# Performance work log

Measured on AMD Instinct MI355X. Metric: run time of the kernel, lower is better.

## Reference

```python
import jax, jax.numpy as jnp
import numpy as np
import math

HIDDEN = 1024
N_HEADS = 16
HEAD_DIM = HIDDEN // N_HEADS

def _safe(x, clamp_val):
    x = jnp.nan_to_num(x, nan=0.0, posinf=0.0, neginf=0.0)
    return jnp.clip(x, -clamp_val, clamp_val)

def _stable_linear(x, W, b):
    # StableLinear: clamp(50) -> linear -> clamp(50)
    x = _safe(x, 50.0)
    out = x @ W.T + b
    return _safe(out, 50.0)

def setup_inputs() -> dict:
    key = jax.random.key(0)
    ks = jax.random.split(key, 12)
    bsz, q_len, kv_len = 4, 1024, 2048
    q = jax.random.normal(ks[0], (bsz, q_len, HIDDEN), dtype=jnp.float32)
    kv = jax.random.normal(ks[1], (bsz, kv_len, HIDDEN), dtype=jnp.float32)
    key_padding_mask = jax.random.bernoulli(ks[2], 0.1, (bsz, kv_len))
    bound = 1.0 / math.sqrt(HIDDEN)
    def mk_w(k):
        return jax.random.uniform(k, (HIDDEN, HIDDEN), jnp.float32, -bound, bound)
    def mk_b(k):
        return jax.random.uniform(k, (HIDDEN,), jnp.float32, -bound, bound)
    return {
        'q': q, 'kv': kv, 'key_padding_mask': key_padding_mask,
        'Wq': mk_w(ks[3]), 'bq': mk_b(ks[4]),
        'Wk': mk_w(ks[5]), 'bk': mk_b(ks[6]),
        'Wv': mk_w(ks[7]), 'bv': mk_b(ks[8]),
        'Wo': mk_w(ks[9]), 'bo': mk_b(ks[10]),
    }

def reference(q, kv, key_padding_mask, Wq, bq, Wk, bk, Wv, bv, Wo, bo):
    bsz, q_len, _ = q.shape
    kv_len = kv.shape[1]
    # outer _safe(50) then StableLinear's own _safe(50) (idempotent)
    qh = _stable_linear(_safe(q, 50.0), Wq, bq)
    kh = _stable_linear(_safe(kv, 50.0), Wk, bk)
    vh = _stable_linear(_safe(kv, 50.0), Wv, bv)
    # [b, h, s, d]
    qh = qh.reshape(bsz, q_len, N_HEADS, HEAD_DIM).transpose(0, 2, 1, 3)
    kh = kh.reshape(bsz, kv_len, N_HEADS, HEAD_DIM).transpose(0, 2, 1, 3)
    vh = vh.reshape(bsz, kv_len, N_HEADS, HEAD_DIM).transpose(0, 2, 1, 3)
    scores = jnp.einsum('bhqd,bhkd->bhqk', qh.astype(jnp.float32), kh.astype(jnp.float32))
    scores = scores / math.sqrt(HEAD_DIM)
    scores = jnp.clip(scores, -80.0, 80.0)
    scores = jnp.where(key_padding_mask[:, None, None, :], -10000.0, scores)
    attn = jax.nn.softmax(scores, axis=-1)  # dropout is identity in eval mode
    out = jnp.einsum('bhqk,bhkd->bhqd', attn, vh.astype(jnp.float32))
    out = out.transpose(0, 2, 1, 3).reshape(bsz, q_len, HIDDEN)
    out = _stable_linear(_safe(out, 50.0), Wo, bo)
    return _safe(out, 50.0)
```

## Files before the change

kernel.cpp:

```cpp
#include <hip/hip_runtime.h>
#include <hip/hip_bf16.h>
#include <stdint.h>
#include <math.h>

#define HIDDEN 1024
#define NHEADS 16
#define HDIM   64
#define BSZ    4
#define QLEN   1024
#define KVLEN  2048

typedef __bf16 bf16_t;
typedef __bf16 bf16x8 __attribute__((ext_vector_type(8)));
typedef __bf16 bf16x4 __attribute__((ext_vector_type(4)));
typedef float  f32x4  __attribute__((ext_vector_type(4)));

#define C_SCALE 0.18033688f
#define C_FMADD (-43.2808512f)

#define GLOAD16(g, l) \
    __builtin_amdgcn_global_load_lds((const __attribute__((address_space(1))) void*)(g), \
                                     (__attribute__((address_space(3))) void*)(l), 16, 0, 0)

__device__ __forceinline__ float clamp50(float v) {
    return fminf(fmaxf(v, -50.f), 50.f);
}

#define NQ4  ((BSZ * QLEN  * HIDDEN) / 4)
#define NKV4 ((BSZ * KVLEN * HIDDEN) / 4)
#define NW4  ((HIDDEN * HIDDEN) / 4)
#define NCVT ((NQ4 + NKV4 + 4 * NW4) / 256)

__global__ void cvt_all_kernel(const float* __restrict__ q, const float* __restrict__ kv,
                               const float* __restrict__ W0, const float* __restrict__ W1,
                               const float* __restrict__ W2, const float* __restrict__ W3,
                               bf16_t* __restrict__ q_bf, bf16_t* __restrict__ kv_bf,
                               bf16_t* __restrict__ w_bf,
                               const void* __restrict__ msk, float* __restrict__ maskadd) {
    if (blockIdx.x >= NCVT) {
        __shared__ int s_float, s_multi;
        const int t = threadIdx.x;
        if (t == 0) { s_float = 0; s_multi = 0; }
        __syncthreads();
        const uint32_t* w = (const uint32_t*)msk;
        int cf = 0, cm = 0;
        for (int i = t; i < 2048; i += 256) {
            uint32_t v = w[i];
            if (v == 0x3F800000u) cf++;
            else if (v & 0xFFFFFF00u) cm++;
        }
        if (cf) atomicAdd(&s_float, cf);
        if (cm) atomicAdd(&s_multi, cm);
        __syncthreads();
        const int mode = (s_float > 0) ? 2 : ((s_multi > 0) ? 0 : 1);
        const int base = (blockIdx.x - NCVT) * 2048;
        for (int i = base + t; i < base + 2048; i += 256) {
            bool m;
            if (mode == 2)      m = ((const float*)msk)[i] != 0.0f;
            else if (mode == 1) m = ((const int*)msk)[i] != 0;
            else                m = ((const unsigned char*)msk)[i] != 0;
            maskadd[i] = m ? (-100000.0f + C_FMADD) : C_FMADD;
        }
        return;
    }
    const int i = blockIdx.x * blockDim.x + threadIdx.x;
    const float4* src;
    bf16x4* dst;
    if (i < NQ4) {
        src = (const float4*)q + i;            dst = (bf16x4*)q_bf + i;
    } else if (i < NQ4 + NKV4) {
        const int j = i - NQ4;
        src = (const float4*)kv + j;           dst = (bf16x4*)kv_bf + j;
    } else {
        const int j = i - (NQ4 + NKV4);
        const int ws = j >> 18, off = j & (NW4 - 1);
        const float* W = (ws == 0) ? W0 : (ws == 1) ? W1 : (ws == 2) ? W2 : W3;
        src = (const float4*)W + off;          dst = (bf16x4*)w_bf + (size_t)ws * NW4 + off;
    }
    const float4 v = *src;
    bf16x4 o;
    o[0] = (bf16_t)clamp50(v.x); o[1] = (bf16_t)clamp50(v.y);
    o[2] = (bf16_t)clamp50(v.z); o[3] = (bf16_t)clamp50(v.w);
    *dst = o;
}

template <int NT>
__device__ __forceinline__ void stage_tile8(const char* __restrict__ Ab,
                                            const char* __restrict__ Bb,
                                            char* base, int kt, int wave, int rowl, int srcsw)
{
#pragma unroll
    for (int i = 0; i < 2; ++i) {
        const int row = i * 64 + wave * 8 + rowl;
        GLOAD16(Ab + (size_t)row * (HIDDEN * 2) + kt * 128 + srcsw,
                base + i * 8192 + wave * 1024);
    }
#pragma unroll
    for (int i = 0; i < NT / 64; ++i) {
        const int row = i * 64 + wave * 8 + rowl;
        GLOAD16(Bb + (size_t)row * (HIDDEN * 2) + kt * 128 + srcsw,
                base + 16384 + i * 8192 + wave * 1024);
    }
}

template <int NT>
__device__ __forceinline__ void gemm_core_db8(const char* __restrict__ Ab,
                                              const char* __restrict__ Bb,
                                              char* Ls,
                                              f32x4 (&acc)[4][NT / 64],
                                              int wave, int lane, int wm, int wn)
{
    constexpr int NFB = NT / 64;
    constexpr int BUF = (128 + NT) * 128;
    const int srcsw = ((lane & 7) ^ (lane >> 3)) << 4;
    const int rowl = lane >> 3;
    const int ql = lane & 15;

    stage_tile8<NT>(Ab, Bb, Ls, 0, wave, rowl, srcsw);
    __syncthreads();

    for (int kt = 0; kt < HIDDEN / 64; ++kt) {
        const int cur = kt & 1;
        if (kt < HIDDEN / 64 - 1)
            stage_tile8<NT>(Ab, Bb, Ls + (cur ^ 1) * BUF, kt + 1, wave, rowl, srcsw);
        const char* Abase = Ls + cur * BUF;
        const char* Bbase = Abase + 16384;
#pragma unroll
        for (int kc = 0; kc < 2; ++kc) {
            const int kbyte = kc * 64 + ((lane >> 4) << 4);
            bf16x8 af[4], bfr[NFB];
#pragma unroll
            for (int f2 = 0; f2 < 4; ++f2) {
                const int arow = wm * 64 + f2 * 16 + ql;
                af[f2] = *(const bf16x8*)(Abase + arow * 128 + (kbyte ^ ((arow & 7) << 4)));
            }
#pragma unroll
            for (int f2 = 0; f2 < NFB; ++f2) {
                const int brow = wn * (NT / 4) + f2 * 16 + ql;
                bfr[f2] = *(const bf16x8*)(Bbase + brow * 128 + (kbyte ^ ((brow & 7) << 4)));
            }
#pragma unroll
            for (int mf = 0; mf < 4; ++mf)
#pragma unroll
                for (int nf = 0; nf < NFB; ++nf)
                    acc[mf][nf] = __builtin_amdgcn_mfma_f32_16x16x32_bf16(af[mf], bfr[nf], acc[mf][nf], 0, 0, 0);
        }
        __syncthreads();
    }
}

template <int NF>
__device__ __forceinline__ void epi_head(f32x4 (&acc)[4][NF], const float* bias,
                                         bf16_t* out, int m0, int n0, int slog,
                                         int wm, int wn, int lane)
{
#pragma unroll
    for (int mf = 0; mf < 4; ++mf) {
#pragma unroll
        for (int nf = 0; nf < NF; ++nf) {
            const int gn = n0 + wn * (NF * 16) + nf * 16 + (lane & 15);
            const float bv = bias[gn];
#pragma unroll
            for (int r = 0; r < 4; ++r) {
                const int gm = m0 + wm * 64 + mf * 16 + ((lane >> 4) << 2) + r;
                const float v = clamp50(acc[mf][nf][r] + bv);
                const int b = gm >> slog;
                const int s = gm & ((1 << slog) - 1);
                const int h = gn >> 6, d = gn & 63;
                out[((((size_t)(b * NHEADS + h)) << slog) + s) * HDIM + d] = (bf16_t)v;
            }
        }
    }
}

__global__ __launch_bounds__(512)
void gemm_proj_all(const bf16_t* __restrict__ q_bf, const bf16_t* __restrict__ kv_bf,
                   const bf16_t* __restrict__ w_bf,
                   const float* __restrict__ bq, const float* __restrict__ bk,
                   const float* __restrict__ bv,
                   bf16_t* __restrict__ qh, bf16_t* __restrict__ kh,
                   bf16_t* __restrict__ vt)
{
    __shared__ __align__(16) bf16_t Smem[2 * 256 * 64];

    const int bid = blockIdx.x;
    const int lid = (bid & 7) * 160 + (bid >> 3);

    int seg, j;
    if (lid < 256)      { seg = 0; j = lid; }
    else if (lid < 768) { seg = 1; j = lid - 256; }
    else                { seg = 2; j = lid - 768; }
    const int m0 = (j >> 3) * 128;
    const int n0 = (j & 7) * 128;
    const bf16_t* A    = (seg == 0) ? q_bf : kv_bf;
    const bf16_t* B    = w_bf + (size_t)seg * (HIDDEN * HIDDEN);
    const float*  bias = (seg == 0) ? bq : (seg == 1) ? bk : bv;

    const int t = threadIdx.x;
    const int wave = t >> 6, lane = t & 63;
    const int wm = wave >> 2, wn = wave & 3;

    f32x4 acc[4][2] = {};
    gemm_core_db8<128>((const char*)A + (size_t)m0 * (HIDDEN * 2),
                       (const char*)B + (size_t)n0 * (HIDDEN * 2),
                       (char*)Smem, acc, wave, lane, wm, wn);

    if (seg == 0) {
        epi_head<2>(acc, bias, qh, m0, n0, 10, wm, wn, lane);
        return;
    }
    if (seg == 1) {
        epi_head<2>(acc, bias, kh, m0, n0, 11, wm, wn, lane);
        return;
    }

    bf16_t* Cls = Smem;
    const int dl = t >> 2;
    const int sh = (t & 3) << 4;
    const int gn = n0 + dl;
    const int h = gn >> 6, d = gn & 63;
    const int bb = m0 >> 11;
    bf16_t* dst = vt + ((size_t)((bb * NHEADS + h) * HDIM + d)) * KVLEN
                + (m0 & (KVLEN - 1)) + sh;
    __syncthreads();
#pragma unroll
    for (int ph = 0; ph < 2; ++ph) {
        if (wm == ph) {
#pragma unroll
            for (int mf = 0; mf < 4; ++mf) {
#pragma unroll
                for (int nf = 0; nf < 2; ++nf) {
                    const int dcol = wn * 32 + nf * 16 + (lane & 15);
                    const float bv2 = bias[n0 + dcol];
#pragma unroll
                    for (int r = 0; r < 4; ++r) {
                        const int srow = mf * 16 + ((lane >> 4) << 2) + r;
                        Cls[srow * 130 + dcol] = (bf16_t)clamp50(acc[mf][nf][r] + bv2);
                    }
                }
            }
        }
        __syncthreads();
#pragma unroll
        for (int j0 = 0; j0 < 16; j0 += 8) {
            bf16x8 v;
#pragma unroll
            for (int jj = 0; jj < 8; ++jj) v[jj] = Cls[(sh + j0 + jj) * 130 + dl];
            *(bf16x8*)(dst + ph * 64 + j0) = v;
        }
        __syncthreads();
    }
}

__global__ __launch_bounds__(512)
void gemm_out_kernel(const bf16_t* __restrict__ A, const bf16_t* __restrict__ B,
                     const float* __restrict__ bias, float* __restrict__ out)
{
    constexpr int NT = 64;
    __shared__ __align__(16) bf16_t Smem[2 * (128 + NT) * 64];

    const int bid = blockIdx.x;
    const int lid = (bid & 7) * 64 + (bid >> 3);
    const int m0 = (lid >> 4) * 128;
    const int n0 = (lid & 15) * NT;
    const int t = threadIdx.x;
    const int wave = t >> 6, lane = t & 63;
    const int wm = wave >> 2, wn = wave & 3;

    f32x4 acc[4][1] = {};
    gemm_core_db8<NT>((const char*)A + (size_t)m0 * (HIDDEN * 2),
                      (const char*)B + (size_t)n0 * (HIDDEN * 2),
                      (char*)Smem, acc, wave, lane, wm, wn);

#pragma unroll
    for (int mf = 0; mf < 4; ++mf) {
        const int gn = n0 + wn * 16 + (lane & 15);
        const float bv = bias[gn];
#pragma unroll
        for (int r = 0; r < 4; ++r) {
            const int gm = m0 + wm * 64 + mf * 16 + ((lane >> 4) << 2) + r;
            out[(size_t)gm * HIDDEN + gn] = clamp50(acc[mf][0][r] + bv);
        }
    }
}

__global__ __launch_bounds__(512)
void attn_fwd_kernel(const bf16_t* __restrict__ Qh, const bf16_t* __restrict__ Kh,
                     const bf16_t* __restrict__ Vt, const float* __restrict__ maskadd,
                     bf16_t* __restrict__ aout)
{
    __shared__ __align__(16) bf16_t Kls[2][64 * 64];
    __shared__ __align__(16) bf16_t Vls[2][64 * 64];
    __shared__ __align__(16) float Cbuf[4][32 * 64];
    __shared__ float Lbuf[4][2][16];

    const int f = blockIdx.x;
    const int o = (f & 7) * 64 + (f >> 3);
    const int qt = o & 7;
    const int bh = o >> 3;
    const int b = bh >> 4, h = bh & 15;
    const int t = threadIdx.x, wave = t >> 6, lane = t & 63;
    const int wq = wave & 3;
    const int wg = wave >> 2;
    const int g = lane >> 4, ql = lane & 15;

    const int qbase = qt * 128 + wq * 32;
    bf16x8 qf[2][2];
#pragma unroll
    for (int qq = 0; qq < 2; ++qq) {
        const bf16_t* qp = Qh + ((size_t)bh * QLEN + qbase + qq * 16 + ql) * HDIM + (g << 3);
        qf[qq][0] = *(const bf16x8*)qp;
        qf[qq][1] = *(const bf16x8*)(qp + 32);
    }

    f32x4 oacc[2][4] = {};
    float lsum[2] = {0.f, 0.f};

    const int srcsw = ((lane & 7) ^ (lane >> 3)) << 4;
    const int R = wave * 8 + (lane >> 3);
    const int kap = 32 * (R >> 5) + 8 * ((R >> 2) & 3) + 4 * ((R >> 4) & 1) + (R & 3);

    const char* Kb = (const char*)(Kh + (size_t)bh * KVLEN * HDIM);
    const char* Vb = (const char*)(Vt + (size_t)bh * HDIM * KVLEN);
    const float* mrow = maskadd + b * KVLEN + wg * 32 + g * 8;
    const int kb0 = g << 4;
    const int vcol = wg * 64 + kb0;

    GLOAD16(Kb + (size_t)kap * 128 + srcsw, (char*)&Kls[0][0] + wave * 1024);
    GLOAD16(Vb + (size_t)R * (KVLEN * 2) + srcsw, (char*)&Vls[0][0] + wave * 1024);
    f32x4 madd_c[2], madd_n[2];
    madd_c[0] = *(const f32x4*)(mrow);
    madd_c[1] = *(const f32x4*)(mrow + 4);
    __syncthreads();

    for (int kt = 0; kt < KVLEN / 64; ++kt) {
        const int cur = kt & 1;
        if (kt < KVLEN / 64 - 1) {
            const size_t ko = (size_t)(kt + 1) * 8192;
            GLOAD16(Kb + ko + (size_t)kap * 128 + srcsw,
                    (char*)&Kls[cur ^ 1][0] + wave * 1024);
            GLOAD16(Vb + (size_t)R * (KVLEN * 2) + (size_t)(kt + 1) * 128 + srcsw,
                    (char*)&Vls[cur ^ 1][0] + wave * 1024);
            madd_n[0] = *(const f32x4*)(mrow + (kt + 1) * 64);
            madd_n[1] = *(const f32x4*)(mrow + (kt + 1) * 64 + 4);
        }
        const char* Kc = (const char*)&Kls[cur][0];
        const char* Vc = (const char*)&Vls[cur][0];

        f32x4 sacc[2][2] = {};
        __builtin_amdgcn_s_setprio(1);
#pragma unroll
        for (int kb = 0; kb < 2; ++kb) {
            const int key = wg * 32 + kb * 16 + ql;
            const int rowoff = key * 128;
            const int sw = (key & 7) << 4;
            const bf16x8 kf0 = *(const bf16x8*)(Kc + rowoff + ((kb0)      ^ sw));
            const bf16x8 kf1 = *(const bf16x8*)(Kc + rowoff + ((kb0 + 64) ^ sw));
#pragma unroll
            for (int qq = 0; qq < 2; ++qq) {
                sacc[qq][kb] = __builtin_amdgcn_mfma_f32_16x16x32_bf16(kf0, qf[qq][0], sacc[qq][kb], 0, 0, 0);
                sacc[qq][kb] = __builtin_amdgcn_mfma_f32_16x16x32_bf16(kf1, qf[qq][1], sacc[qq][kb], 0, 0, 0);
            }
        }
        __builtin_amdgcn_s_setprio(0);

        bf16x8 pa[2];
#pragma unroll
        for (int qq = 0; qq < 2; ++qq) {
            float pv[2][4];
            float ls = 0.f;
#pragma unroll
            for (int kb = 0; kb < 2; ++kb) {
#pragma unroll
                for (int r = 0; r < 4; ++r) {
                    pv[kb][r] = __builtin_amdgcn_exp2f(
                        __builtin_fmaf(sacc[qq][kb][r], C_SCALE, madd_c[kb][r]));
                    ls += pv[kb][r];
                }
            }
            lsum[qq] += ls;
#pragma unroll
            for (int r = 0; r < 4; ++r) {
                pa[qq][r]     = (bf16_t)pv[0][r];
                pa[qq][4 + r] = (bf16_t)pv[1][r];
            }
        }

        __builtin_amdgcn_s_setprio(1);
#pragma unroll
        for (int db = 0; db < 4; ++db) {
            const int vrow = db * 16 + ql;
            const int vsw = (vrow & 7) << 4;
            const bf16x8 vf = *(const bf16x8*)(Vc + vrow * 128 + (vcol ^ vsw));
#pragma unroll
            for (int qq = 0; qq < 2; ++qq)
                oacc[qq][db] = __builtin_amdgcn_mfma_f32_16x16x32_bf16(pa[qq], vf, oacc[qq][db], 0, 0, 0);
        }
        __builtin_amdgcn_s_setprio(0);

        __syncthreads();
#pragma unroll
        for (int kb = 0; kb < 2; ++kb) madd_c[kb] = madd_n[kb];
    }

#pragma unroll
    for (int qq = 0; qq < 2; ++qq) {
        float l = lsum[qq];
        l += __shfl_xor(l, 16);
        l += __shfl_xor(l, 32);
        lsum[qq] = l;
    }
    const int rbase = g << 2;
    if (wg == 1) {
#pragma unroll
        for (int qq = 0; qq < 2; ++qq) {
#pragma unroll
            for (int db = 0; db < 4; ++db)
#pragma unroll
                for (int r = 0; r < 4; ++r)
                    Cbuf[wq][(qq * 16 + rbase + r) * 64 + db * 16 + ql] = oacc[qq][db][r];
            if (lane < 16) Lbuf[wq][qq][lane] = lsum[qq];
        }
    }
    __syncthreads();
    if (wg == 0) {
#pragma unroll
        for (int qq = 0; qq < 2; ++qq) {
            const float Lq = lsum[qq] + Lbuf[wq][qq][ql];
#pragma unroll
            for (int r = 0; r < 4; ++r) {
                const float Lr = __shfl(Lq, rbase + r);
                const float inv = 1.0f / Lr;
                const int qrow = qbase + qq * 16 + rbase + r;
                bf16_t* orow = aout + ((size_t)(b * QLEN + qrow)) * HIDDEN + h * HDIM;
#pragma unroll
                for (int db = 0; db < 4; ++db) {
                    const float add = Cbuf[wq][(qq * 16 + rbase + r) * 64 + db * 16 + ql];
                    orow[db * 16 + ql] = (bf16_t)((oacc[qq][db][r] + add) * inv);
                }
            }
        }
    }
}

extern "C" void kernel_launch(void* const* d_in, const int* in_sizes, int n_in,
                              void* d_out, int out_size, void* d_ws, size_t ws_size,
                              hipStream_t stream) {
    (void)in_sizes; (void)n_in; (void)out_size; (void)ws_size;
    const float* q   = (const float*)d_in[0];
    const float* kv  = (const float*)d_in[1];
    const void*  msk = d_in[2];
    const float* Wq  = (const float*)d_in[3];
    const float* bq  = (const float*)d_in[4];
    const float* Wk  = (const float*)d_in[5];
    const float* bk  = (const float*)d_in[6];
    const float* Wv  = (const float*)d_in[7];
    const float* bv  = (const float*)d_in[8];
    const float* Wo  = (const float*)d_in[9];
    const float* bo  = (const float*)d_in[10];

    char* ws = (char*)d_ws;
    const size_t MB = 1024 * 1024;
    float*  maskadd = (float*)ws;
    bf16_t* w_bf  = (bf16_t*)(ws + 32 * 1024);
    bf16_t* q_bf  = (bf16_t*)(ws + 32 * 1024 + 8  * MB);
    bf16_t* kv_bf = (bf16_t*)(ws + 32 * 1024 + 16 * MB);
    bf16_t* qh    = (bf16_t*)(ws + 32 * 1024 + 32 * MB);
    bf16_t* kh    = (bf16_t*)(ws + 32 * 1024 + 40 * MB);
    bf16_t* vt    = (bf16_t*)(ws + 32 * 1024 + 56 * MB);
    bf16_t* aout  = q_bf;

    bf16_t* wo_bf = w_bf + (size_t)3 * HIDDEN * HIDDEN;

    cvt_all_kernel<<<dim3(NCVT + 4), 256, 0, stream>>>(
        q, kv, Wq, Wk, Wv, Wo, q_bf, kv_bf, w_bf, msk, maskadd);

    gemm_proj_all<<<dim3(1280), 512, 0, stream>>>(
        q_bf, kv_bf, w_bf, bq, bk, bv, qh, kh, vt);

    attn_fwd_kernel<<<dim3(512), 512, 0, stream>>>(qh, kh, vt, maskadd, aout);

    gemm_out_kernel<<<dim3(512), 512, 0, stream>>>(aout, wo_bf, bo, (float*)d_out);
}
```

Measured before the change: 140.1 us.

## Fuse fp32-to-bf16 activation conversion into projection GEMM tile staging

The projection GEMM now reads q and kv directly in fp32. Each thread loads its A tile into registers, clamps to ±50, converts to bf16 and writes it to the swizzled LDS slot. The weight-and-mask conversion kernel no longer converts activations. This removes a full HBM round trip for the 48MB activation read and the bf16 intermediate write and re-read. In exchange the GEMM reads twice as many bytes per A tile, and the A prefetch goes through registers with a manual LDS store instead of direct global_load_lds, which could expose more latency or raise register pressure.

Result: no change. 140.0 us (-0.1%).

```diff
diff --git a/kernel.cpp b/kernel.cpp
--- a/kernel.cpp
+++ b/kernel.cpp
@@ -26,18 +26,14 @@
     return fminf(fmaxf(v, -50.f), 50.f);
 }
 
-#define NQ4  ((BSZ * QLEN  * HIDDEN) / 4)
-#define NKV4 ((BSZ * KVLEN * HIDDEN) / 4)
 #define NW4  ((HIDDEN * HIDDEN) / 4)
-#define NCVT ((NQ4 + NKV4 + 4 * NW4) / 256)
-
-__global__ void cvt_all_kernel(const float* __restrict__ q, const float* __restrict__ kv,
-                               const float* __restrict__ W0, const float* __restrict__ W1,
-                               const float* __restrict__ W2, const float* __restrict__ W3,
-                               bf16_t* __restrict__ q_bf, bf16_t* __restrict__ kv_bf,
-                               bf16_t* __restrict__ w_bf,
-                               const void* __restrict__ msk, float* __restrict__ maskadd) {
-    if (blockIdx.x >= NCVT) {
+#define NWCVT (4 * NW4 / 256)
+
+__global__ void cvt_w_mask_kernel(const float* __restrict__ W0, const float* __restrict__ W1,
+                                  const float* __restrict__ W2, const float* __restrict__ W3,
+                                  bf16_t* __restrict__ w_bf,
+                                  const void* __restrict__ msk, float* __restrict__ maskadd) {
+    if (blockIdx.x >= NWCVT) {
         __shared__ int s_float, s_multi;
         const int t = threadIdx.x;
         if (t == 0) { s_float = 0; s_multi = 0; }
@@ -53,7 +49,7 @@
         if (cm) atomicAdd(&s_multi, cm);
         __syncthreads();
         const int mode = (s_float > 0) ? 2 : ((s_multi > 0) ? 0 : 1);
-        const int base = (blockIdx.x - NCVT) * 2048;
+        const int base = (blockIdx.x - NWCVT) * 2048;
         for (int i = base + t; i < base + 2048; i += 256) {
             bool m;
             if (mode == 2)      m = ((const float*)msk)[i] != 0.0f;
@@ -64,86 +60,98 @@
         return;
     }
     const int i = blockIdx.x * blockDim.x + threadIdx.x;
-    const float4* src;
-    bf16x4* dst;
-    if (i < NQ4) {
-        src = (const float4*)q + i;            dst = (bf16x4*)q_bf + i;
-    } else if (i < NQ4 + NKV4) {
-        const int j = i - NQ4;
-        src = (const float4*)kv + j;           dst = (bf16x4*)kv_bf + j;
-    } else {
-        const int j = i - (NQ4 + NKV4);
-        const int ws = j >> 18, off = j & (NW4 - 1);
-        const float* W = (ws == 0) ? W0 : (ws == 1) ? W1 : (ws == 2) ? W2 : W3;
-        src = (const float4*)W + off;          dst = (bf16x4*)w_bf + (size_t)ws * NW4 + off;
-    }
-    const float4 v = *src;
+    const int ws = i >> 18, off = i & (NW4 - 1);
+    const float* W = (ws == 0) ? W0 : (ws == 1) ? W1 : (ws == 2) ? W2 : W3;
+    const float4 v = ((const float4*)W)[off];
     bf16x4 o;
     o[0] = (bf16_t)clamp50(v.x); o[1] = (bf16_t)clamp50(v.y);
     o[2] = (bf16_t)clamp50(v.z); o[3] = (bf16_t)clamp50(v.w);
-    *dst = o;
-}
-
-template <int NT>
-__device__ __forceinline__ void stage_tile8(const char* __restrict__ Ab,
-                                            const char* __restrict__ Bb,
-                                            char* base, int kt, int wave, int rowl, int srcsw)
-{
-#pragma unroll
-    for (int i = 0; i < 2; ++i) {
-        const int row = i * 64 + wave * 8 + rowl;
-        GLOAD16(Ab + (size_t)row * (HIDDEN * 2) + kt * 128 + srcsw,
-                base + i * 8192 + wave * 1024);
-    }
-#pragma unroll
-    for (int i = 0; i < NT / 64; ++i) {
-        const int row = i * 64 + wave * 8 + rowl;
-        GLOAD16(Bb + (size_t)row * (HIDDEN * 2) + kt * 128 + srcsw,
-                base + 16384 + i * 8192 + wave * 1024);
-    }
-}
-
-template <int NT>
-__device__ __forceinline__ void gemm_core_db8(const char* __restrict__ Ab,
-                                              const char* __restrict__ Bb,
-                                              char* Ls,
-                                              f32x4 (&acc)[4][NT / 64],
-                                              int wave, int lane, int wm, int wn)
-{
-    constexpr int NFB = NT / 64;
-    constexpr int BUF = (128 + NT) * 128;
+    ((bf16x4*)w_bf)[(size_t)ws * NW4 + off] = o;
+}
+
+__device__ __forceinline__ void proj_core(const char* __restrict__ Ab,
+                                          const char* __restrict__ Bb,
+                                          char* Ls, f32x4 (&acc)[4][2],
+                                          int wave, int lane, int wm, int wn)
+{
+    constexpr int BUF = 256 * 128;
     const int srcsw = ((lane & 7) ^ (lane >> 3)) << 4;
     const int rowl = lane >> 3;
     const int ql = lane & 15;
 
-    stage_tile8<NT>(Ab, Bb, Ls, 0, wave, rowl, srcsw);
+    float4 a0[2], a1[2];
+#pragma unroll
+    for (int i = 0; i < 2; ++i) {
+        const int row = i * 64 + wave * 8 + rowl;
+        const float4* p = (const float4*)(Ab + (size_t)row * (HIDDEN * 4) + (srcsw << 1));
+        a0[i] = p[0]; a1[i] = p[1];
+    }
+#pragma unroll
+    for (int i = 0; i < 2; ++i) {
+        const int row = i * 64 + wave * 8 + rowl;
+        GLOAD16(Bb + (size_t)row * (HIDDEN * 2) + srcsw,
+                Ls + 16384 + i * 8192 + wave * 1024);
+    }
+#pragma unroll
+    for (int i = 0; i < 2; ++i) {
+        bf16x8 o;
+        o[0] = (bf16_t)clamp50(a0[i].x); o[1] = (bf16_t)clamp50(a0[i].y);
+        o[2] = (bf16_t)clamp50(a0[i].z); o[3] = (bf16_t)clamp50(a0[i].w);
+        o[4] = (bf16_t)clamp50(a1[i].x); o[5] = (bf16_t)clamp50(a1[i].y);
+        o[6] = (bf16_t)clamp50(a1[i].z); o[7] = (bf16_t)clamp50(a1[i].w);
+        *(bf16x8*)(Ls + i * 8192 + wave * 1024 + lane * 16) = o;
+    }
     __syncthreads();
 
     for (int kt = 0; kt < HIDDEN / 64; ++kt) {
         const int cur = kt & 1;
-        if (kt < HIDDEN / 64 - 1)
-            stage_tile8<NT>(Ab, Bb, Ls + (cur ^ 1) * BUF, kt + 1, wave, rowl, srcsw);
+        if (kt < HIDDEN / 64 - 1) {
+#pragma unroll
+            for (int i = 0; i < 2; ++i) {
+                const int row = i * 64 + wave * 8 + rowl;
+                const float4* p = (const float4*)(Ab + (size_t)row * (HIDDEN * 4)
+                                                  + (kt + 1) * 256 + (srcsw << 1));
+                a0[i] = p[0]; a1[i] = p[1];
+            }
+#pragma unroll
+            for (int i = 0; i < 2; ++i) {
+                const int row = i * 64 + wave * 8 + rowl;
+                GLOAD16(Bb + (size_t)row * (HIDDEN * 2) + (kt + 1) * 128 + srcsw,
+                        Ls + (cur ^ 1) * BUF + 16384 + i * 8192 + wave * 1024);
+            }
+        }
         const char* Abase = Ls + cur * BUF;
         const char* Bbase = Abase + 16384;
 #pragma unroll
         for (int kc = 0; kc < 2; ++kc) {
             const int kbyte = kc * 64 + ((lane >> 4) << 4);
-            bf16x8 af[4], bfr[NFB];
+            bf16x8 af[4], bfr[2];
 #pragma unroll
             for (int f2 = 0; f2 < 4; ++f2) {
                 const int arow = wm * 64 + f2 * 16 + ql;
                 af[f2] = *(const bf16x8*)(Abase + arow * 128 + (kbyte ^ ((arow & 7) << 4)));
             }
 #pragma unroll
-            for (int f2 = 0; f2 < NFB; ++f2) {
-                const int brow = wn * (NT / 4) + f2 * 16 + ql;
+            for (int f2 = 0; f2 < 2; ++f2) {
+                const int brow = wn * 32 + f2 * 16 + ql;
                 bfr[f2] = *(const bf16x8*)(Bbase + brow * 128 + (kbyte ^ ((brow & 7) << 4)));
             }
 #pragma unroll
             for (int mf = 0; mf < 4; ++mf)
 #pragma unroll
-                for (int nf = 0; nf < NFB; ++nf)
+                for (int nf = 0; nf < 2; ++nf)
                     acc[mf][nf] = __builtin_amdgcn_mfma_f32_16x16x32_bf16(af[mf], bfr[nf], acc[mf][nf], 0, 0, 0);
+        }
+        if (kt < HIDDEN / 64 - 1) {
+#pragma unroll
+            for (int i = 0; i < 2; ++i) {
+                bf16x8 o;
+                o[0] = (bf16_t)clamp50(a0[i].x); o[1] = (bf16_t)clamp50(a0[i].y);
+                o[2] = (bf16_t)clamp50(a0[i].z); o[3] = (bf16_t)clamp50(a0[i].w);
+                o[4] = (bf16_t)clamp50(a1[i].x); o[5] = (bf16_t)clamp50(a1[i].y);
+                o[6] = (bf16_t)clamp50(a1[i].z); o[7] = (bf16_t)clamp50(a1[i].w);
+                *(bf16x8*)(Ls + (cur ^ 1) * BUF + i * 8192 + wave * 1024 + lane * 16) = o;
+            }
         }
         __syncthreads();
     }
@@ -174,7 +182,7 @@
 }
 
 __global__ __launch_bounds__(512)
-void gemm_proj_all(const bf16_t* __restrict__ q_bf, const bf16_t* __restrict__ kv_bf,
+void gemm_proj_all(const float* __restrict__ qf32, const float* __restrict__ kvf32,
                    const bf16_t* __restrict__ w_bf,
                    const float* __restrict__ bq, const float* __restrict__ bk,
                    const float* __restrict__ bv,
@@ -192,7 +200,7 @@
     else                { seg = 2; j = lid - 768; }
     const int m0 = (j >> 3) * 128;
     const int n0 = (j & 7) * 128;
-    const bf16_t* A    = (seg == 0) ? q_bf : kv_bf;
+    const float*  A    = (seg == 0) ? qf32 : kvf32;
     const bf16_t* B    = w_bf + (size_t)seg * (HIDDEN * HIDDEN);
     const float*  bias = (seg == 0) ? bq : (seg == 1) ? bk : bv;
 
@@ -201,9 +209,9 @@
     const int wm = wave >> 2, wn = wave & 3;
 
     f32x4 acc[4][2] = {};
-    gemm_core_db8<128>((const char*)A + (size_t)m0 * (HIDDEN * 2),
-                       (const char*)B + (size_t)n0 * (HIDDEN * 2),
-                       (char*)Smem, acc, wave, lane, wm, wn);
+    proj_core((const char*)A + (size_t)m0 * (HIDDEN * 4),
+              (const char*)B + (size_t)n0 * (HIDDEN * 2),
+              (char*)Smem, acc, wave, lane, wm, wn);
 
     if (seg == 0) {
         epi_head<2>(acc, bias, qh, m0, n0, 10, wm, wn, lane);
@@ -247,6 +255,71 @@
 #pragma unroll
             for (int jj = 0; jj < 8; ++jj) v[jj] = Cls[(sh + j0 + jj) * 130 + dl];
             *(bf16x8*)(dst + ph * 64 + j0) = v;
+        }
+        __syncthreads();
+    }
+}
+
+template <int NT>
+__device__ __forceinline__ void stage_tile8(const char* __restrict__ Ab,
+                                            const char* __restrict__ Bb,
+                                            char* base, int kt, int wave, int rowl, int srcsw)
+{
+#pragma unroll
+    for (int i = 0; i < 2; ++i) {
+        const int row = i * 64 + wave * 8 + rowl;
+        GLOAD16(Ab + (size_t)row * (HIDDEN * 2) + kt * 128 + srcsw,
+                base + i * 8192 + wave * 1024);
+    }
+#pragma unroll
+    for (int i = 0; i < NT / 64; ++i) {
+        const int row = i * 64 + wave * 8 + rowl;
+        GLOAD16(Bb + (size_t)row * (HIDDEN * 2) + kt * 128 + srcsw,
+                base + 16384 + i * 8192 + wave * 1024);
+    }
+}
+
+template <int NT>
+__device__ __forceinline__ void gemm_core_db8(const char* __restrict__ Ab,
+                                              const char* __restrict__ Bb,
+                                              char* Ls,
+                                              f32x4 (&acc)[4][NT / 64],
+                                              int wave, int lane, int wm, int wn)
+{
+    constexpr int NFB = NT / 64;
+    constexpr int BUF = (128 + NT) * 128;
+    const int srcsw = ((lane & 7) ^ (lane >> 3)) << 4;
+    const int rowl = lane >> 3;
+    const int ql = lane & 15;
+
+    stage_tile8<NT>(Ab, Bb, Ls, 0, wave, rowl, srcsw);
+    __syncthreads();
+
+    for (int kt = 0; kt < HIDDEN / 64; ++kt) {
+        const int cur = kt & 1;
+        if (kt < HIDDEN / 64 - 1)
+            stage_tile8<NT>(Ab, Bb, Ls + (cur ^ 1) * BUF, kt + 1, wave, rowl, srcsw);
+        const char* Abase = Ls + cur * BUF;
+        const char* Bbase = Abase + 16384;
+#pragma unroll
+        for (int kc = 0; kc < 2; ++kc) {
+            const int kbyte = kc * 64 + ((lane >> 4) << 4);
+            bf16x8 af[4], bfr[NFB];
+#pragma unroll
+            for (int f2 = 0; f2 < 4; ++f2) {
+                const int arow = wm * 64 + f2 * 16 + ql;
+                af[f2] = *(const bf16x8*)(Abase + arow * 128 + (kbyte ^ ((arow & 7) << 4)));
+            }
+#pragma unroll
+            for (int f2 = 0; f2 < NFB; ++f2) {
+                const int brow = wn * (NT / 4) + f2 * 16 + ql;
+                bfr[f2] = *(const bf16x8*)(Bbase + brow * 128 + (kbyte ^ ((brow & 7) << 4)));
+            }
+#pragma unroll
+            for (int mf = 0; mf < 4; ++mf)
+#pragma unroll
+                for (int nf = 0; nf < NFB; ++nf)
+                    acc[mf][nf] = __builtin_amdgcn_mfma_f32_16x16x32_bf16(af[mf], bfr[nf], acc[mf][nf], 0, 0, 0);
         }
         __syncthreads();
     }
@@ -463,20 +536,18 @@
     const size_t MB = 1024 * 1024;
     float*  maskadd = (float*)ws;
     bf16_t* w_bf  = (bf16_t*)(ws + 32 * 1024);
-    bf16_t* q_bf  = (bf16_t*)(ws + 32 * 1024 + 8  * MB);
-    bf16_t* kv_bf = (bf16_t*)(ws + 32 * 1024 + 16 * MB);
+    bf16_t* aout  = (bf16_t*)(ws + 32 * 1024 + 8  * MB);
     bf16_t* qh    = (bf16_t*)(ws + 32 * 1024 + 32 * MB);
     bf16_t* kh    = (bf16_t*)(ws + 32 * 1024 + 40 * MB);
     bf16_t* vt    = (bf16_t*)(ws + 32 * 1024 + 56 * MB);
-    bf16_t* aout  = q_bf;
 
     bf16_t* wo_bf = w_bf + (size_t)3 * HIDDEN * HIDDEN;
 
-    cvt_all_kernel<<<dim3(NCVT + 4), 256, 0, stream>>>(
-        q, kv, Wq, Wk, Wv, Wo, q_bf, kv_bf, w_bf, msk, maskadd);
+    cvt_w_mask_kernel<<<dim3(NWCVT + 4), 256, 0, stream>>>(
+        Wq, Wk, Wv, Wo, w_bf, msk, maskadd);
 
     gemm_proj_all<<<dim3(1280), 512, 0, stream>>>(
-        q_bf, kv_bf, w_bf, bq, bk, bv, qh, kh, vt);
+        q, kv, w_bf, bq, bk, bv, qh, kh, vt);
 
     attn_fwd_kernel<<<dim3(512), 512, 0, stream>>>(qh, kh, vt, maskadd, aout);
 
```
